# Optimization experiments

Hardware: AMD Instinct MI355X
Metric: run time of the kernel (lower is better)

The kernel has to match this reference:

```python
import jax, jax.numpy as jnp
import numpy as np

QUANT_LIMIT = 127.0  # 2**(8-1) - 1, signed int8


def _quantize(x, amax):
    # per-tensor symmetric int8 quantization: round(clip(x * 127/amax, -127, 127))
    s = QUANT_LIMIT / amax
    return jnp.round(jnp.clip(x * s, -QUANT_LIMIT, QUANT_LIMIT))


def setup_inputs() -> dict:
    key = jax.random.key(0)
    kx, kw, kb = jax.random.split(key, 3)
    B, S, K, N = 4, 2048, 4096, 4096
    x = jax.random.normal(kx, (B, S, K), dtype=jnp.float32)
    weight = jax.random.normal(kw, (N, K), dtype=jnp.float32) * 0.03  # kaiming-ish scale
    bias = jax.random.normal(kb, (N,), dtype=jnp.float32) * 0.01
    amax = jnp.float32(4.0)     # calibrated activation amax for N(0,1)
    amax_w = jnp.float32(0.12)  # calibrated weight amax
    return {"x": x, "weight": weight, "bias": bias, "amax": amax, "amax_w": amax_w}


def reference(x, weight, bias, amax, amax_w):
    # quantize to int8
    qx = _quantize(x, amax).astype(jnp.int8)           # [B,S,K]
    qw = _quantize(weight, amax_w).astype(jnp.int8)    # [N,K]
    # int8 matmul with int32 accumulation (exact-accumulation variant of the
    # approximate-multiplier kernel)
    acc = jnp.einsum("bsk,nk->bsn", qx.astype(jnp.int32), qw.astype(jnp.int32))
    # rescale: output = acc / ((127/amax) * (127/amax_w)), then bias add
    scale = (QUANT_LIMIT / amax) * (QUANT_LIMIT / amax_w)
    out = acc.astype(jnp.float32) / scale + bias
    return out
```

## Files before the change

### kernel.cpp

```cpp
#include <hip/hip_runtime.h>
#include <hip/hip_bf16.h>
#include <stdint.h>

typedef __attribute__((ext_vector_type(4))) int i32x4;

#define QLIM 127.0f
#define BM 128
#define BN 128
#define BK 64

__device__ __forceinline__ int quant_pack4(float4 v, float s) {
    float a0 = rintf(fminf(fmaxf(v.x * s, -QLIM), QLIM));
    float a1 = rintf(fminf(fmaxf(v.y * s, -QLIM), QLIM));
    float a2 = rintf(fminf(fmaxf(v.z * s, -QLIM), QLIM));
    float a3 = rintf(fminf(fmaxf(v.w * s, -QLIM), QLIM));
    return ((int)a0 & 255) | (((int)a1 & 255) << 8) |
           (((int)a2 & 255) << 16) | (((int)a3 & 255) << 24);
}

__global__ void quantize_kernel(const float* __restrict__ in, int4* __restrict__ q,
                                const float* __restrict__ amax, long n16) {
    const float s = QLIM / amax[0];
    const long stride = (long)gridDim.x * blockDim.x;
    for (long i = (long)blockIdx.x * blockDim.x + threadIdx.x; i < n16; i += stride) {
        const float4* p = (const float4*)in + i * 4;
        float4 v0 = p[0], v1 = p[1], v2 = p[2], v3 = p[3];
        int4 r;
        r.x = quant_pack4(v0, s);
        r.y = quant_pack4(v1, s);
        r.z = quant_pack4(v2, s);
        r.w = quant_pack4(v3, s);
        q[i] = r;
    }
}

__global__ __launch_bounds__(256) void gemm_i8_kernel(
    const signed char* __restrict__ A,
    const signed char* __restrict__ B,
    const float* __restrict__ bias,
    const float* __restrict__ amax,
    const float* __restrict__ amax_w,
    float* __restrict__ C,
    int M, int N, int K)
{
    __shared__ signed char As[BM * BK];
    __shared__ signed char Bs[BN * BK];

    const int tid  = threadIdx.x;
    const int wid  = tid >> 6;
    const int lane = tid & 63;
    const int wm   = wid >> 1;
    const int wn   = wid & 1;
    const int bm   = blockIdx.y;
    const int bn   = blockIdx.x;

    const int srow = tid >> 2;
    const int scol = (tid & 3) << 4;

    const signed char* a_base = A + (size_t)(bm * BM) * K;
    const signed char* b_base = B + (size_t)(bn * BN) * K;

    const int fr = lane & 15;
    const int fk = (lane >> 4) << 4;

    i32x4 acc[4][4] = {};

    for (int k0 = 0; k0 < K; k0 += BK) {
#pragma unroll
        for (int j = 0; j < 2; ++j) {
            const signed char* ag = a_base + (size_t)(j * 64 + srow) * K + k0 + scol;
            const signed char* bg = b_base + (size_t)(j * 64 + srow) * K + k0 + scol;
            __builtin_amdgcn_global_load_lds(
                (const __attribute__((address_space(1))) void*)ag,
                (__attribute__((address_space(3))) void*)(As + j * 4096 + wid * 1024),
                16, 0, 0);
            __builtin_amdgcn_global_load_lds(
                (const __attribute__((address_space(1))) void*)bg,
                (__attribute__((address_space(3))) void*)(Bs + j * 4096 + wid * 1024),
                16, 0, 0);
        }
        __syncthreads();

        i32x4 a_frag[4], b_frag[4];
#pragma unroll
        for (int m = 0; m < 4; ++m)
            a_frag[m] = *(const i32x4*)(As + (wm * 64 + m * 16 + fr) * 64 + fk);
#pragma unroll
        for (int n = 0; n < 4; ++n)
            b_frag[n] = *(const i32x4*)(Bs + (wn * 64 + n * 16 + fr) * 64 + fk);

#pragma unroll
        for (int m = 0; m < 4; ++m)
#pragma unroll
            for (int n = 0; n < 4; ++n)
                acc[m][n] = __builtin_amdgcn_mfma_i32_16x16x64_i8(
                    a_frag[m], b_frag[n], acc[m][n], 0, 0, 0);

        __syncthreads();
    }

    const float sa  = QLIM / amax[0];
    const float sw  = QLIM / amax_w[0];
    const float inv = 1.0f / (sa * sw);
    const int row0 = bm * BM + wm * 64;
    const int col0 = bn * BN + wn * 64;
#pragma unroll
    for (int m = 0; m < 4; ++m) {
#pragma unroll
        for (int n = 0; n < 4; ++n) {
            const int colc = col0 + n * 16 + fr;
            const float bv = bias[colc];
#pragma unroll
            for (int r = 0; r < 4; ++r) {
                const int rowc = row0 + m * 16 + ((lane >> 4) << 2) + r;
                C[(size_t)rowc * N + colc] = (float)acc[m][n][r] * inv + bv;
            }
        }
    }
}

extern "C" void kernel_launch(void* const* d_in, const int* in_sizes, int n_in,
                              void* d_out, int out_size, void* d_ws, size_t ws_size,
                              hipStream_t stream) {
    const float* x      = (const float*)d_in[0];
    const float* w      = (const float*)d_in[1];
    const float* bias   = (const float*)d_in[2];
    const float* amax   = (const float*)d_in[3];
    const float* amax_w = (const float*)d_in[4];
    float* out = (float*)d_out;

    const int N = in_sizes[2];
    const int K = in_sizes[1] / N;
    const int M = in_sizes[0] / K;

    signed char* qx = (signed char*)d_ws;
    signed char* qw = qx + (size_t)M * K;

    const long nx16 = (long)M * K / 16;
    const long nw16 = (long)N * K / 16;
    quantize_kernel<<<2048, 256, 0, stream>>>(x, (int4*)qx, amax, nx16);
    quantize_kernel<<<1024, 256, 0, stream>>>(w, (int4*)qw, amax_w, nw16);

    dim3 grid(N / BN, M / BM);
    gemm_i8_kernel<<<grid, 256, 0, stream>>>(qx, qw, bias, amax, amax_w, out, M, N, K);
}
```

Baseline: 442.3 us.

## Double GEMM K-tile, swizzle block order, and coalesce quantize loads

The GEMM K tile grows from 64 to 128 bytes, which halves the number of barrier-separated iterations and runs two MFMA sub-steps per staged tile. Blocks are launched on a 1D grid and remapped with an XCD-style swizzle (bid&7) so that neighbouring tiles share L2 locality. The quantize kernel now has each thread process one float4 and emit one int, which gives coalesced adjacent accesses. The costs are double the LDS use (32KB) and a possible rise in LDS bank conflicts, since the row stride is now 128 bytes.

```diff
diff --git a/kernel.cpp b/kernel.cpp
--- a/kernel.cpp
+++ b/kernel.cpp
@@ -1,5 +1,4 @@
 #include <hip/hip_runtime.h>
-#include <hip/hip_bf16.h>
 #include <stdint.h>
 
 typedef __attribute__((ext_vector_type(4))) int i32x4;
@@ -7,7 +6,7 @@
 #define QLIM 127.0f
 #define BM 128
 #define BN 128
-#define BK 64
+#define BKB 128
 
 __device__ __forceinline__ int quant_pack4(float4 v, float s) {
     float a0 = rintf(fminf(fmaxf(v.x * s, -QLIM), QLIM));
@@ -18,20 +17,12 @@
            (((int)a2 & 255) << 16) | (((int)a3 & 255) << 24);
 }
 
-__global__ void quantize_kernel(const float* __restrict__ in, int4* __restrict__ q,
-                                const float* __restrict__ amax, long n16) {
+__global__ void quantize_kernel(const float4* __restrict__ in, int* __restrict__ q,
+                                const float* __restrict__ amax, long n4) {
     const float s = QLIM / amax[0];
     const long stride = (long)gridDim.x * blockDim.x;
-    for (long i = (long)blockIdx.x * blockDim.x + threadIdx.x; i < n16; i += stride) {
-        const float4* p = (const float4*)in + i * 4;
-        float4 v0 = p[0], v1 = p[1], v2 = p[2], v3 = p[3];
-        int4 r;
-        r.x = quant_pack4(v0, s);
-        r.y = quant_pack4(v1, s);
-        r.z = quant_pack4(v2, s);
-        r.w = quant_pack4(v3, s);
-        q[i] = r;
-    }
+    for (long i = (long)blockIdx.x * blockDim.x + threadIdx.x; i < n4; i += stride)
+        q[i] = quant_pack4(in[i], s);
 }
 
 __global__ __launch_bounds__(256) void gemm_i8_kernel(
@@ -43,19 +34,25 @@
     float* __restrict__ C,
     int M, int N, int K)
 {
-    __shared__ signed char As[BM * BK];
-    __shared__ signed char Bs[BN * BK];
+    __shared__ signed char As[BM * BKB];
+    __shared__ signed char Bs[BN * BKB];
 
     const int tid  = threadIdx.x;
     const int wid  = tid >> 6;
     const int lane = tid & 63;
     const int wm   = wid >> 1;
     const int wn   = wid & 1;
-    const int bm   = blockIdx.y;
-    const int bn   = blockIdx.x;
 
-    const int srow = tid >> 2;
-    const int scol = (tid & 3) << 4;
+    const int nwg = gridDim.x;
+    const int cpx = nwg >> 3;
+    const int bid = (int)blockIdx.x;
+    const int swz = (bid & 7) * cpx + (bid >> 3);
+    const int ntn = N / BN;
+    const int bm  = swz / ntn;
+    const int bn  = swz % ntn;
+
+    const int srow = tid >> 3;
+    const int scol = (tid & 7) << 4;
 
     const signed char* a_base = A + (size_t)(bm * BM) * K;
     const signed char* b_base = B + (size_t)(bn * BN) * K;
@@ -65,11 +62,11 @@
 
     i32x4 acc[4][4] = {};
 
-    for (int k0 = 0; k0 < K; k0 += BK) {
+    for (int k0 = 0; k0 < K; k0 += BKB) {
 #pragma unroll
-        for (int j = 0; j < 2; ++j) {
-            const signed char* ag = a_base + (size_t)(j * 64 + srow) * K + k0 + scol;
-            const signed char* bg = b_base + (size_t)(j * 64 + srow) * K + k0 + scol;
+        for (int j = 0; j < 4; ++j) {
+            const signed char* ag = a_base + (size_t)(j * 32 + srow) * K + k0 + scol;
+            const signed char* bg = b_base + (size_t)(j * 32 + srow) * K + k0 + scol;
             __builtin_amdgcn_global_load_lds(
                 (const __attribute__((address_space(1))) void*)ag,
                 (__attribute__((address_space(3))) void*)(As + j * 4096 + wid * 1024),
@@ -81,21 +78,23 @@
         }
         __syncthreads();
 
-        i32x4 a_frag[4], b_frag[4];
 #pragma unroll
-        for (int m = 0; m < 4; ++m)
-            a_frag[m] = *(const i32x4*)(As + (wm * 64 + m * 16 + fr) * 64 + fk);
+        for (int kk = 0; kk < 2; ++kk) {
+            i32x4 a_frag[4], b_frag[4];
 #pragma unroll
-        for (int n = 0; n < 4; ++n)
-            b_frag[n] = *(const i32x4*)(Bs + (wn * 64 + n * 16 + fr) * 64 + fk);
+            for (int m = 0; m < 4; ++m)
+                a_frag[m] = *(const i32x4*)(As + (wm * 64 + m * 16 + fr) * BKB + kk * 64 + fk);
+#pragma unroll
+            for (int n = 0; n < 4; ++n)
+                b_frag[n] = *(const i32x4*)(Bs + (wn * 64 + n * 16 + fr) * BKB + kk * 64 + fk);
 
 #pragma unroll
-        for (int m = 0; m < 4; ++m)
+            for (int m = 0; m < 4; ++m)
 #pragma unroll
-            for (int n = 0; n < 4; ++n)
-                acc[m][n] = __builtin_amdgcn_mfma_i32_16x16x64_i8(
-                    a_frag[m], b_frag[n], acc[m][n], 0, 0, 0);
-
+                for (int n = 0; n < 4; ++n)
+                    acc[m][n] = __builtin_amdgcn_mfma_i32_16x16x64_i8(
+                        a_frag[m], b_frag[n], acc[m][n], 0, 0, 0);
+        }
         __syncthreads();
     }
 
@@ -136,11 +135,11 @@
     signed char* qx = (signed char*)d_ws;
     signed char* qw = qx + (size_t)M * K;
 
-    const long nx16 = (long)M * K / 16;
-    const long nw16 = (long)N * K / 16;
-    quantize_kernel<<<2048, 256, 0, stream>>>(x, (int4*)qx, amax, nx16);
-    quantize_kernel<<<1024, 256, 0, stream>>>(w, (int4*)qw, amax_w, nw16);
+    const long nx4 = (long)M * K / 4;
+    const long nw4 = (long)N * K / 4;
+    quantize_kernel<<<2048, 256, 0, stream>>>((const float4*)x, (int*)qx, amax, nx4);
+    quantize_kernel<<<1024, 256, 0, stream>>>((const float4*)w, (int*)qw, amax_w, nw4);
 
-    dim3 grid(N / BN, M / BM);
-    gemm_i8_kernel<<<grid, 256, 0, stream>>>(qx, qw, bias, amax, amax_w, out, M, N, K);
+    const int nblocks = (M / BM) * (N / BN);
+    gemm_i8_kernel<<<nblocks, 256, 0, stream>>>(qx, qw, bias, amax, amax_w, out, M, N, K);
 }
```

Measured after the change: 478.6 us. +8.2%, slower.
